# Kernel tuning notes

Hardware: AMD Instinct MI355X
Metric: run time of the kernel (lower is better)

The kernel has to match this reference:

```python
import jax, jax.numpy as jnp
import numpy as np

EMBED = 1024
HEADS = 16
HEAD_DIM = EMBED // HEADS


def setup_inputs() -> dict:
    key = jax.random.key(0)
    ks = jax.random.split(key, 8)
    N, L = 2, 2048
    s = 0.02
    return {
        "values": jax.random.normal(ks[0], (N, L, EMBED), jnp.float32),
        "keys": jax.random.normal(ks[1], (N, L, EMBED), jnp.float32),
        "queries": jax.random.normal(ks[2], (N, L, EMBED), jnp.float32),
        "Wv": jax.random.normal(ks[3], (HEAD_DIM, HEAD_DIM), jnp.float32) * s,
        "Wk": jax.random.normal(ks[4], (HEAD_DIM, HEAD_DIM), jnp.float32) * s,
        "Wq": jax.random.normal(ks[5], (HEAD_DIM, HEAD_DIM), jnp.float32) * s,
        "Wo": jax.random.normal(ks[6], (EMBED, EMBED), jnp.float32) * s,
        "bo": jnp.zeros((EMBED,), jnp.float32),
    }


def reference(values, keys, queries, Wv, Wk, Wq, Wo, bo):
    N, Lq = queries.shape[0], queries.shape[1]
    Lk = keys.shape[1]
    Lv = values.shape[1]
    # split heads: [N, L, H, D]
    v = values.reshape(N, Lv, HEADS, HEAD_DIM)
    k = keys.reshape(N, Lk, HEADS, HEAD_DIM)
    q = queries.reshape(N, Lq, HEADS, HEAD_DIM)
    # per-head linear projections (torch Linear: x @ W.T), shared across heads
    v = jnp.einsum('nlhd,ed->nlhe', v, Wv)
    k = jnp.einsum('nlhd,ed->nlhe', k, Wk)
    q = jnp.einsum('nlhd,ed->nlhe', q, Wq)
    # attention scores [N, H, Lq, Lk]
    scores = jnp.einsum('nqhd,nkhd->nhqk', q, k) / jnp.sqrt(jnp.float32(HEAD_DIM))
    attn = jax.nn.softmax(scores, axis=-1)
    out = jnp.einsum('nhql,nlhd->nqhd', attn, v).reshape(N, Lq, EMBED)
    return out @ Wo.T + bo
```

## Files before the change

### kernel.cpp

```cpp
#include <hip/hip_runtime.h>
#include <hip/hip_bf16.h>
#include <cstdint>
#include <cstddef>

#define HEADS 16
#define HDIM  64
#define EMBED 1024
#define SEQ   2048
#define NB    2

typedef __attribute__((ext_vector_type(8))) short short8;
typedef __attribute__((ext_vector_type(4))) short s16x4;
typedef __attribute__((ext_vector_type(4))) float f32x4;
typedef __attribute__((ext_vector_type(16))) float f32x16;

__device__ __forceinline__ short f2bf(float f) {
    union { float f; uint32_t u; } in{f};
    uint32_t u = in.u;
    u += 0x7fffu + ((u >> 16) & 1u);
    return (short)(u >> 16);
}

__device__ __forceinline__ int cvtpk(float a, float b) {
    __hip_bfloat162 h = __float22bfloat162_rn(make_float2(a, b));
    int i;
    __builtin_memcpy(&i, &h, 4);
    return i;
}

__device__ __forceinline__ short8 load_cvt8(const float* __restrict__ p) {
    const f32x4* q = (const f32x4*)p;
    f32x4 v0 = q[0], v1 = q[1];
    short8 r;
    r[0] = f2bf(v0[0]); r[1] = f2bf(v0[1]); r[2] = f2bf(v0[2]); r[3] = f2bf(v0[3]);
    r[4] = f2bf(v1[0]); r[5] = f2bf(v1[1]); r[6] = f2bf(v1[2]); r[7] = f2bf(v1[3]);
    return r;
}

__global__ __launch_bounds__(256) void wcvt_kernel(
    const float* __restrict__ Wq, const float* __restrict__ Wk,
    const float* __restrict__ Wv, const float* __restrict__ Wo,
    short* __restrict__ Wqb, short* __restrict__ Wkb,
    short* __restrict__ Wvb, short* __restrict__ Wob) {
    int b = blockIdx.x, tid = threadIdx.x;
    if (b < 1024) {
        int o = b * 1024 + tid * 4;
        int page = o >> 9, inp = o & 511;
        int nb = page >> 5, kb = page & 31;
        int lp = inp >> 3, jj = inp & 7;
        int row = nb * 16 + (lp & 15);
        int colf = kb * 32 + (lp >> 4) * 8 + jj;
        f32x4 v = *(const f32x4*)(Wo + row * 1024 + colf);
        s16x4 r;
        r[0] = f2bf(v[0]); r[1] = f2bf(v[1]); r[2] = f2bf(v[2]); r[3] = f2bf(v[3]);
        *(s16x4*)(Wob + o) = r;
    } else {
        const float* src = (b == 1024) ? Wq : (b == 1025) ? Wk : Wv;
        short* dst = (b == 1024) ? Wqb : (b == 1025) ? Wkb : Wvb;
        float scale = (b == 1024) ? 0.125f * 1.44269504088896341f : 1.0f;
#pragma unroll
        for (int k = 0; k < 4; ++k) {
            int idx = tid * 16 + k * 4;
            f32x4 v = *(const f32x4*)(src + idx);
            s16x4 r;
            r[0] = f2bf(v[0] * scale); r[1] = f2bf(v[1] * scale);
            r[2] = f2bf(v[2] * scale); r[3] = f2bf(v[3] * scale);
            *(s16x4*)(dst + idx) = r;
        }
    }
}

__global__ __launch_bounds__(256) void proj_kernel(
    const float* __restrict__ qrys, const float* __restrict__ keys,
    const float* __restrict__ vals,
    const short* __restrict__ Wqb, const short* __restrict__ Wkb,
    const short* __restrict__ Wvb,
    short* __restrict__ Qp, short* __restrict__ Kf, short* __restrict__ Vf) {
    __shared__ short tile[64][72];
    int tid = threadIdx.x, lane = tid & 63, w = tid >> 6;
    int g = lane >> 4, c = lane & 15;
    int tt = blockIdx.x * 64;
    int h = blockIdx.y;
    int z = blockIdx.z;
    int op = z >> 1, n = z & 1;
    int nh = n * 16 + h;
    const float* src = (op == 0) ? qrys : (op == 1) ? keys : vals;
    const short* Wb = (op == 0) ? Wqb : (op == 1) ? Wkb : Wvb;

    int lt0 = tt + w * 16;
    const float* sp_ = src + ((size_t)(n * SEQ + lt0 + c) * 16 + h) * 64;
    short8 a0 = load_cvt8(sp_ + 8 * g);
    short8 a1 = load_cvt8(sp_ + 32 + 8 * g);
#pragma unroll
    for (int ot = 0; ot < 4; ++ot) {
        short8 b0 = *(const short8*)(Wb + (ot * 16 + c) * 64 + 8 * g);
        short8 b1 = *(const short8*)(Wb + (ot * 16 + c) * 64 + 32 + 8 * g);
        f32x4 acc = {0.f, 0.f, 0.f, 0.f};
        acc = __builtin_amdgcn_mfma_f32_16x16x32_bf16(a0, b0, acc, 0, 0, 0);
        acc = __builtin_amdgcn_mfma_f32_16x16x32_bf16(a1, b1, acc, 0, 0, 0);
        if (op == 2) {
#pragma unroll
            for (int r = 0; r < 4; ++r)
                tile[ot * 16 + c][w * 16 + 4 * g + r] = f2bf(acc[r]);
        } else {
#pragma unroll
            for (int r = 0; r < 4; ++r)
                tile[w * 16 + 4 * g + r][ot * 16 + c] = f2bf(acc[r]);
        }
    }
    __syncthreads();
    if (op == 0) {
#pragma unroll
        for (int it = 0; it < 2; ++it) {
            int idx = tid + it * 256;
            int row = idx >> 3, ch = idx & 7;
            short8 v = *(const short8*)(&tile[row][ch * 8]);
            *(short8*)(Qp + ((size_t)nh * SEQ + tt + row) * 64 + ch * 8) = v;
        }
    } else {
        short* dst = (op == 1) ? Kf : Vf;
        int spx = tt >> 10;
        int tbase = (tt >> 5) & 31;
        size_t grp = (size_t)(nh * 2 + spx) * 32;
#pragma unroll
        for (int it = 0; it < 2; ++it) {
            int idx = tid + it * 256;
            int tl2 = idx >> 8;
            int p = (idx >> 6) & 3;
            int ln = idx & 63;
            int hi2 = ln >> 5, col2 = ln & 31;
            const short* srcp;
            if (op == 1) {
                srcp = &tile[tl2 * 32 + col2][p * 16 + hi2 * 8];
            } else {
                srcp = &tile[(p & 1) * 32 + col2][tl2 * 32 + (p >> 1) * 16 + hi2 * 8];
            }
            *(short8*)(dst + ((grp + tbase + tl2) * 4 + p) * 512 + ln * 8) =
                *(const short8*)srcp;
        }
    }
}

__global__ __launch_bounds__(256, 3) void attn_kernel(
    const short* __restrict__ Qp, const short* __restrict__ Kf,
    const short* __restrict__ Vf, short* __restrict__ X) {
    __shared__ float obuf[2][32][64];
    __shared__ float larr[2][2][32];

    int tid = threadIdx.x, lane = tid & 63, wave = tid >> 6;
    int col = lane & 31, hi = lane >> 5;
    int qg = wave >> 1, sp = wave & 1;

    int lid = blockIdx.x;
    int xcd = lid & 7, idx = lid >> 3;
    int nh = xcd * 4 + (idx & 3);
    int qb = idx >> 2;
    int n = nh >> 4, h = nh & 15;
    int q0w = qb * 64 + qg * 32;

    const short* Qb = Qp + (size_t)nh * SEQ * 64;
    const short* Kw = Kf + (((size_t)(nh * 2 + sp)) << 16) + lane * 8;
    const short* Vw = Vf + (((size_t)(nh * 2 + sp)) << 16) + lane * 8;

    short8 qf[4];
#pragma unroll
    for (int t = 0; t < 4; ++t)
        qf[t] = *(const short8*)(Qb + (size_t)(q0w + col) * 64 + 16 * t + 8 * hi);

    f32x16 o0, o1;
#pragma unroll
    for (int r = 0; r < 16; ++r) { o0[r] = 0.f; o1[r] = 0.f; }
    float la = 0.f, lb = 0.f;

#define LOADT(t, kf, vf)                                                       \
    {                                                                          \
        _Pragma("unroll")                                                      \
        for (int dt = 0; dt < 4; ++dt)                                         \
            kf[dt] = *(const short8*)(Kw + ((size_t)((t) * 4 + dt) << 9));     \
        _Pragma("unroll")                                                      \
        for (int p = 0; p < 4; ++p)                                            \
            vf[p] = *(const short8*)(Vw + ((size_t)((t) * 4 + p) << 9));       \
    }

#define COMPUTE(kf, vf)                                                        \
    {                                                                          \
        f32x16 s;                                                              \
        _Pragma("unroll")                                                      \
        for (int r = 0; r < 16; ++r) s[r] = 0.f;                               \
        __builtin_amdgcn_s_setprio(1);                                         \
        _Pragma("unroll")                                                      \
        for (int dt = 0; dt < 4; ++dt)                                         \
            s = __builtin_amdgcn_mfma_f32_32x32x16_bf16(kf[dt], qf[dt], s, 0, 0, 0); \
        __builtin_amdgcn_s_setprio(0);                                         \
        _Pragma("unroll")                                                      \
        for (int r = 0; r < 16; r += 2) {                                      \
            s[r] = __builtin_amdgcn_exp2f(s[r]);                               \
            s[r + 1] = __builtin_amdgcn_exp2f(s[r + 1]);                       \
            la += s[r];                                                        \
            lb += s[r + 1];                                                    \
        }                                                                      \
        int pk0 = cvtpk(s[0], s[1]),   pk1 = cvtpk(s[2], s[3]);                \
        int pk2 = cvtpk(s[4], s[5]),   pk3 = cvtpk(s[6], s[7]);                \
        int pk4 = cvtpk(s[8], s[9]),   pk5 = cvtpk(s[10], s[11]);              \
        int pk6 = cvtpk(s[12], s[13]), pk7 = cvtpk(s[14], s[15]);              \
        auto r02 = __builtin_amdgcn_permlane32_swap(pk0, pk2, false, false);   \
        auto r13 = __builtin_amdgcn_permlane32_swap(pk1, pk3, false, false);   \
        auto r46 = __builtin_amdgcn_permlane32_swap(pk4, pk6, false, false);   \
        auto r57 = __builtin_amdgcn_permlane32_swap(pk5, pk7, false, false);   \
        union { int i[4]; short8 s8; } pa0, pa1;                               \
        pa0.i[0] = r02[0]; pa0.i[1] = r13[0]; pa0.i[2] = r02[1]; pa0.i[3] = r13[1]; \
        pa1.i[0] = r46[0]; pa1.i[1] = r57[0]; pa1.i[2] = r46[1]; pa1.i[3] = r57[1]; \
        __builtin_amdgcn_s_setprio(1);                                         \
        o0 = __builtin_amdgcn_mfma_f32_32x32x16_bf16(pa0.s8, vf[0], o0, 0, 0, 0); \
        o1 = __builtin_amdgcn_mfma_f32_32x32x16_bf16(pa0.s8, vf[1], o1, 0, 0, 0); \
        o0 = __builtin_amdgcn_mfma_f32_32x32x16_bf16(pa1.s8, vf[2], o0, 0, 0, 0); \
        o1 = __builtin_amdgcn_mfma_f32_32x32x16_bf16(pa1.s8, vf[3], o1, 0, 0, 0); \
        __builtin_amdgcn_s_setprio(0);                                         \
    }

    short8 kfA[4], kfB[4];
    short8 vfA[4], vfB[4];
    LOADT(0, kfA, vfA);
#pragma unroll 1
    for (int t = 0; t < 32; t += 2) {
        LOADT(t + 1, kfB, vfB);
        COMPUTE(kfA, vfA);
        if (t + 2 < 32) LOADT(t + 2, kfA, vfA);
        COMPUTE(kfB, vfB);
    }
#undef LOADT
#undef COMPUTE

    float l_loc = la + lb;
    l_loc += __shfl_xor(l_loc, 32);

    if (lane < 32) larr[qg][sp][col] = l_loc;
    if (sp == 0) {
#pragma unroll
        for (int r = 0; r < 16; ++r) {
            int rq = (r & 3) + 8 * (r >> 2) + 4 * hi;
            obuf[qg][rq][col] = o0[r];
            obuf[qg][rq][32 + col] = o1[r];
        }
    }
    __syncthreads();
    if (sp == 1) {
#pragma unroll
        for (int r = 0; r < 16; ++r) {
            int rq = (r & 3) + 8 * (r >> 2) + 4 * hi;
            float ltot = larr[qg][0][rq] + larr[qg][1][rq];
            float iv = 1.0f / ltot;
            float v0 = o0[r] + obuf[qg][rq][col];
            float v1 = o1[r] + obuf[qg][rq][32 + col];
            int m = n * SEQ + q0w + rq;
            size_t base = (((size_t)(m >> 4) * 32 + h * 2) << 9) +
                          (size_t)(m & 15) * 8 + ((col >> 3) << 7) + (col & 7);
            X[base] = f2bf(v0 * iv);
            X[base + 512] = f2bf(v1 * iv);
        }
    }
}

__global__ __launch_bounds__(256) void ogemm_kernel(
    const short* __restrict__ Xf, const short* __restrict__ Wf,
    const float* __restrict__ bo, float* __restrict__ out) {
    int tid = threadIdx.x, lane = tid & 63, wave = tid >> 6;
    int g = lane >> 4, c = lane & 15;
    int wr = wave >> 1, wc = wave & 1;
    int m0 = blockIdx.x * 128 + wr * 64;
    int n0 = blockIdx.y * 64 + wc * 32;

    f32x4 acc[4][2];
#pragma unroll
    for (int i = 0; i < 4; ++i)
#pragma unroll
        for (int j = 0; j < 2; ++j) acc[i][j] = (f32x4){0.f, 0.f, 0.f, 0.f};

    const short* Xp = Xf + (((size_t)(blockIdx.x * 8 + wr * 4) * 32) << 9) + lane * 8;
    const short* Wp = Wf + (((size_t)(blockIdx.y * 4 + wc * 2) * 32) << 9) + lane * 8;

    short8 a[4], b[2];
#pragma unroll
    for (int i = 0; i < 4; ++i) a[i] = *(const short8*)(Xp + ((size_t)i * 32 << 9));
#pragma unroll
    for (int j = 0; j < 2; ++j) b[j] = *(const short8*)(Wp + ((size_t)j * 32 << 9));

    for (int s = 1; s <= 32; ++s) {
        short8 an[4], bn[2];
        if (s < 32) {
#pragma unroll
            for (int i = 0; i < 4; ++i)
                an[i] = *(const short8*)(Xp + (((size_t)i * 32 + s) << 9));
#pragma unroll
            for (int j = 0; j < 2; ++j)
                bn[j] = *(const short8*)(Wp + (((size_t)j * 32 + s) << 9));
        }
#pragma unroll
        for (int i = 0; i < 4; ++i)
#pragma unroll
            for (int j = 0; j < 2; ++j)
                acc[i][j] = __builtin_amdgcn_mfma_f32_16x16x32_bf16(a[i], b[j], acc[i][j], 0, 0, 0);
        if (s < 32) {
#pragma unroll
            for (int i = 0; i < 4; ++i) a[i] = an[i];
#pragma unroll
            for (int j = 0; j < 2; ++j) b[j] = bn[j];
        }
    }

    float bias[2] = {bo[n0 + c], bo[n0 + 16 + c]};
#pragma unroll
    for (int i = 0; i < 4; ++i)
#pragma unroll
        for (int j = 0; j < 2; ++j)
#pragma unroll
            for (int r = 0; r < 4; ++r)
                out[(size_t)(m0 + i * 16 + 4 * g + r) * EMBED + n0 + j * 16 + c] =
                    acc[i][j][r] + bias[j];
}

extern "C" void kernel_launch(void* const* d_in, const int* in_sizes, int n_in,
                              void* d_out, int out_size, void* d_ws, size_t ws_size,
                              hipStream_t stream) {
    const float* vals = (const float*)d_in[0];
    const float* keys = (const float*)d_in[1];
    const float* qrys = (const float*)d_in[2];
    const float* Wv = (const float*)d_in[3];
    const float* Wk = (const float*)d_in[4];
    const float* Wq = (const float*)d_in[5];
    const float* Wo = (const float*)d_in[6];
    const float* bo = (const float*)d_in[7];
    float* out = (float*)d_out;

    char* ws = (char*)d_ws;
    const size_t sz_bf = (size_t)NB * HEADS * SEQ * HDIM * sizeof(short);
    short* Qp = (short*)(ws);
    short* Kf = (short*)(ws + sz_bf);
    short* Vf = (short*)(ws + 2 * sz_bf);
    short* X = (short*)(ws + 3 * sz_bf);
    short* Wob = (short*)(ws + 4 * sz_bf);
    short* Wqb = (short*)(ws + 4 * sz_bf + 2 * 1024 * 1024);
    short* Wkb = Wqb + 64 * 64;
    short* Wvb = Wkb + 64 * 64;

    wcvt_kernel<<<dim3(1027), dim3(256), 0, stream>>>(Wq, Wk, Wv, Wo, Wqb, Wkb, Wvb, Wob);
    proj_kernel<<<dim3(SEQ / 64, HEADS, 6), dim3(256), 0, stream>>>(
        qrys, keys, vals, Wqb, Wkb, Wvb, Qp, Kf, Vf);
    attn_kernel<<<dim3(1024), dim3(256), 0, stream>>>(Qp, Kf, Vf, X);
    ogemm_kernel<<<dim3(NB * SEQ / 128, EMBED / 64), dim3(256), 0, stream>>>(X, Wob, bo, out);
}
```

Before: 95.82 us.

## Stage K/V tiles through LDS with async global_load_lds double buffering

Previously each of the two query-group waves loaded the same K and V fragments directly from global memory into registers. Now the two waves sharing a key split cooperatively stage one tile into a double-buffered LDS area (one wave loads K, the other V) using direct global-to-LDS loads, then all waves read their fragments from LDS. This halves global/L2 traffic for K/V and frees registers, but adds a block-wide barrier and a full vmcnt wait every iteration. The LDS buffer is also reused for the final cross-split reduction.

```diff
diff --git a/kernel.cpp b/kernel.cpp
--- a/kernel.cpp
+++ b/kernel.cpp
@@ -144,8 +144,7 @@
 __global__ __launch_bounds__(256, 3) void attn_kernel(
     const short* __restrict__ Qp, const short* __restrict__ Kf,
     const short* __restrict__ Vf, short* __restrict__ X) {
-    __shared__ float obuf[2][32][64];
-    __shared__ float larr[2][2][32];
+    __shared__ short kv[2][2][8][512];
 
     int tid = threadIdx.x, lane = tid & 63, wave = tid >> 6;
     int col = lane & 31, hi = lane >> 5;
@@ -159,8 +158,9 @@
     int q0w = qb * 64 + qg * 32;
 
     const short* Qb = Qp + (size_t)nh * SEQ * 64;
-    const short* Kw = Kf + (((size_t)(nh * 2 + sp)) << 16) + lane * 8;
-    const short* Vw = Vf + (((size_t)(nh * 2 + sp)) << 16) + lane * 8;
+    const short* Kw = Kf + (((size_t)(nh * 2 + sp)) << 16);
+    const short* Vw = Vf + (((size_t)(nh * 2 + sp)) << 16);
+    const short* Gsrc = (qg ? Vw : Kw) + lane * 8;
 
     short8 qf[4];
 #pragma unroll
@@ -172,14 +172,16 @@
     for (int r = 0; r < 16; ++r) { o0[r] = 0.f; o1[r] = 0.f; }
     float la = 0.f, lb = 0.f;
 
-#define LOADT(t, kf, vf)                                                       \
+#define STAGE(t, b)                                                            \
     {                                                                          \
-        _Pragma("unroll")                                                      \
-        for (int dt = 0; dt < 4; ++dt)                                         \
-            kf[dt] = *(const short8*)(Kw + ((size_t)((t) * 4 + dt) << 9));     \
+        const short* gs_ = Gsrc + (((size_t)(t) * 4) << 9);                    \
+        short* ds_ = &kv[b][sp][qg * 4][0] + lane * 8;                         \
         _Pragma("unroll")                                                      \
         for (int p = 0; p < 4; ++p)                                            \
-            vf[p] = *(const short8*)(Vw + ((size_t)((t) * 4 + p) << 9));       \
+            __builtin_amdgcn_global_load_lds(                                  \
+                (const __attribute__((address_space(1))) void*)(gs_ + (p << 9)), \
+                (__attribute__((address_space(3))) void*)(ds_ + (p << 9)),     \
+                16, 0, 0);                                                     \
     }
 
 #define COMPUTE(kf, vf)                                                        \
@@ -218,29 +220,40 @@
         __builtin_amdgcn_s_setprio(0);                                         \
     }
 
-    short8 kfA[4], kfB[4];
-    short8 vfA[4], vfB[4];
-    LOADT(0, kfA, vfA);
+    STAGE(0, 0);
+    asm volatile("s_waitcnt vmcnt(0)" ::: "memory");
+    __builtin_amdgcn_s_barrier();
+
 #pragma unroll 1
-    for (int t = 0; t < 32; t += 2) {
-        LOADT(t + 1, kfB, vfB);
-        COMPUTE(kfA, vfA);
-        if (t + 2 < 32) LOADT(t + 2, kfA, vfA);
-        COMPUTE(kfB, vfB);
-    }
-#undef LOADT
+    for (int t = 0; t < 32; ++t) {
+        int b = t & 1;
+        short8 kf[4], vf[4];
+#pragma unroll
+        for (int p = 0; p < 4; ++p)
+            kf[p] = *(const short8*)(&kv[b][sp][p][0] + lane * 8);
+#pragma unroll
+        for (int p = 0; p < 4; ++p)
+            vf[p] = *(const short8*)(&kv[b][sp][4 + p][0] + lane * 8);
+        if (t + 1 < 32) STAGE(t + 1, b ^ 1);
+        COMPUTE(kf, vf);
+        asm volatile("s_waitcnt vmcnt(0)" ::: "memory");
+        __builtin_amdgcn_s_barrier();
+    }
+#undef STAGE
 #undef COMPUTE
 
     float l_loc = la + lb;
     l_loc += __shfl_xor(l_loc, 32);
 
-    if (lane < 32) larr[qg][sp][col] = l_loc;
+    float* ob = (float*)&kv[0][0][0][0];
+    float* la_ = (float*)((char*)&kv[0][0][0][0] + 16384);
+    if (lane < 32) la_[(qg * 2 + sp) * 32 + col] = l_loc;
     if (sp == 0) {
 #pragma unroll
         for (int r = 0; r < 16; ++r) {
             int rq = (r & 3) + 8 * (r >> 2) + 4 * hi;
-            obuf[qg][rq][col] = o0[r];
-            obuf[qg][rq][32 + col] = o1[r];
+            ob[(qg * 32 + rq) * 64 + col] = o0[r];
+            ob[(qg * 32 + rq) * 64 + 32 + col] = o1[r];
         }
     }
     __syncthreads();
@@ -248,10 +261,10 @@
 #pragma unroll
         for (int r = 0; r < 16; ++r) {
             int rq = (r & 3) + 8 * (r >> 2) + 4 * hi;
-            float ltot = larr[qg][0][rq] + larr[qg][1][rq];
+            float ltot = la_[qg * 64 + rq] + la_[qg * 64 + 32 + rq];
             float iv = 1.0f / ltot;
-            float v0 = o0[r] + obuf[qg][rq][col];
-            float v1 = o1[r] + obuf[qg][rq][32 + col];
+            float v0 = o0[r] + ob[(qg * 32 + rq) * 64 + col];
+            float v1 = o1[r] + ob[(qg * 32 + rq) * 64 + 32 + col];
             int m = n * SEQ + q0w + rq;
             size_t base = (((size_t)(m >> 4) * 32 + h * 2) << 9) +
                           (size_t)(m & 15) * 8 + ((col >> 3) << 7) + (col & 7);
```

Result: no change. 97.00 us (+1.2%).

## Split attention keys four ways per block with 32-query blocks

Applied to the files above, without the earlier changes.

Each attention block now handles 32 queries instead of 64, and its four waves each take a quarter of the key sequence instead of two query groups times two key halves. The grid doubles to 2048 blocks and the partial outputs and row sums from four waves are reduced through shared memory. This is meant to raise parallelism and shorten each wave's serial key loop. The cost is twice as many K/V loads per query overall and a heavier shared-memory reduction.

```diff
diff --git a/kernel.cpp b/kernel.cpp
--- a/kernel.cpp
+++ b/kernel.cpp
@@ -144,28 +144,31 @@
 __global__ __launch_bounds__(256, 3) void attn_kernel(
     const short* __restrict__ Qp, const short* __restrict__ Kf,
     const short* __restrict__ Vf, short* __restrict__ X) {
-    __shared__ float obuf[2][32][64];
-    __shared__ float larr[2][2][32];
+    __shared__ float ob3[3][32][64];
+    __shared__ float la4[4][32];
 
     int tid = threadIdx.x, lane = tid & 63, wave = tid >> 6;
     int col = lane & 31, hi = lane >> 5;
-    int qg = wave >> 1, sp = wave & 1;
+    int sp = wave;
 
     int lid = blockIdx.x;
     int xcd = lid & 7, idx = lid >> 3;
     int nh = xcd * 4 + (idx & 3);
     int qb = idx >> 2;
     int n = nh >> 4, h = nh & 15;
-    int q0w = qb * 64 + qg * 32;
+    int q0 = qb * 32;
 
     const short* Qb = Qp + (size_t)nh * SEQ * 64;
-    const short* Kw = Kf + (((size_t)(nh * 2 + sp)) << 16) + lane * 8;
-    const short* Vw = Vf + (((size_t)(nh * 2 + sp)) << 16) + lane * 8;
+    int spx = sp >> 1, toff = (sp & 1) * 16;
+    const short* Kw = Kf + (((size_t)(nh * 2 + spx)) << 16) +
+                      (((size_t)toff * 4) << 9) + lane * 8;
+    const short* Vw = Vf + (((size_t)(nh * 2 + spx)) << 16) +
+                      (((size_t)toff * 4) << 9) + lane * 8;
 
     short8 qf[4];
 #pragma unroll
     for (int t = 0; t < 4; ++t)
-        qf[t] = *(const short8*)(Qb + (size_t)(q0w + col) * 64 + 16 * t + 8 * hi);
+        qf[t] = *(const short8*)(Qb + (size_t)(q0 + col) * 64 + 16 * t + 8 * hi);
 
     f32x16 o0, o1;
 #pragma unroll
@@ -222,10 +225,10 @@
     short8 vfA[4], vfB[4];
     LOADT(0, kfA, vfA);
 #pragma unroll 1
-    for (int t = 0; t < 32; t += 2) {
+    for (int t = 0; t < 16; t += 2) {
         LOADT(t + 1, kfB, vfB);
         COMPUTE(kfA, vfA);
-        if (t + 2 < 32) LOADT(t + 2, kfA, vfA);
+        if (t + 2 < 16) LOADT(t + 2, kfA, vfA);
         COMPUTE(kfB, vfB);
     }
 #undef LOADT
@@ -234,25 +237,26 @@
     float l_loc = la + lb;
     l_loc += __shfl_xor(l_loc, 32);
 
-    if (lane < 32) larr[qg][sp][col] = l_loc;
-    if (sp == 0) {
+    if (lane < 32) la4[sp][col] = l_loc;
+    if (sp > 0) {
 #pragma unroll
         for (int r = 0; r < 16; ++r) {
             int rq = (r & 3) + 8 * (r >> 2) + 4 * hi;
-            obuf[qg][rq][col] = o0[r];
-            obuf[qg][rq][32 + col] = o1[r];
+            ob3[sp - 1][rq][col] = o0[r];
+            ob3[sp - 1][rq][32 + col] = o1[r];
         }
     }
     __syncthreads();
-    if (sp == 1) {
+    if (sp == 0) {
 #pragma unroll
         for (int r = 0; r < 16; ++r) {
             int rq = (r & 3) + 8 * (r >> 2) + 4 * hi;
-            float ltot = larr[qg][0][rq] + larr[qg][1][rq];
+            float ltot = la4[0][rq] + la4[1][rq] + la4[2][rq] + la4[3][rq];
             float iv = 1.0f / ltot;
-            float v0 = o0[r] + obuf[qg][rq][col];
-            float v1 = o1[r] + obuf[qg][rq][32 + col];
-            int m = n * SEQ + q0w + rq;
+            float v0 = o0[r] + ob3[0][rq][col] + ob3[1][rq][col] + ob3[2][rq][col];
+            float v1 = o1[r] + ob3[0][rq][32 + col] + ob3[1][rq][32 + col] +
+                       ob3[2][rq][32 + col];
+            int m = n * SEQ + q0 + rq;
             size_t base = (((size_t)(m >> 4) * 32 + h * 2) << 9) +
                           (size_t)(m & 15) * 8 + ((col >> 3) << 7) + (col & 7);
             X[base] = f2bf(v0 * iv);
@@ -346,6 +350,6 @@
     wcvt_kernel<<<dim3(1027), dim3(256), 0, stream>>>(Wq, Wk, Wv, Wo, Wqb, Wkb, Wvb, Wob);
     proj_kernel<<<dim3(SEQ / 64, HEADS, 6), dim3(256), 0, stream>>>(
         qrys, keys, vals, Wqb, Wkb, Wvb, Qp, Kf, Vf);
-    attn_kernel<<<dim3(1024), dim3(256), 0, stream>>>(Qp, Kf, Vf, X);
+    attn_kernel<<<dim3(2048), dim3(256), 0, stream>>>(Qp, Kf, Vf, X);
     ogemm_kernel<<<dim3(NB * SEQ / 128, EMBED / 64), dim3(256), 0, stream>>>(X, Wob, bo, out);
 }
```

After: 98.58 us. +2.9%, slower.
